# Kernel optimization log

Hardware: AMD Instinct MI355X
Metric: run time of the kernel (lower is better)

The kernel has to match this reference:

```python
import jax, jax.numpy as jnp
import numpy as np

INF = 1.0e10
EPS = 1e-12

def setup_inputs() -> dict:
    key = jax.random.key(0)
    k1, k2 = jax.random.split(key)
    B, N, A = 512, 16384, 64
    return {
        "residue_ca_pos": jax.random.normal(k1, (B, N, 3), dtype=jnp.float32) * 10.0,
        "residue_mask": jnp.ones((B, N), dtype=jnp.float32),
        "atom_pos": jax.random.normal(k2, (B, A, 3), dtype=jnp.float32) * 10.0,
        "atom_mask": jnp.ones((B, A), dtype=jnp.float32),
        "max_p": 1,
        "top_k": 4096,
    }

def reference(residue_ca_pos, residue_mask, atom_pos, atom_mask, max_p, top_k):
    # ligand centroid per batch: [B, 3]
    centroid = atom_pos.sum(-2) / atom_mask.sum(-1, keepdims=True)
    # distance from centroid to each residue Ca, invalid residues pushed to +inf
    diff = centroid[:, None, :] - residue_ca_pos            # [B, N, 3]
    dists = jnp.sqrt(jnp.sum(diff * diff, axis=-1) + EPS) + (1.0 - residue_mask) * INF
    # k smallest distances -> neighbor indices [B, top_k]
    _, nbr_indices = jax.lax.top_k(-dists, top_k)
    rows = jnp.arange(residue_mask.shape[0])[:, None]       # [B, 1]
    # scatter writes building the masks (faithful to torch scatter_ with constants)
    residue_spatial_mask = residue_mask.at[rows, nbr_indices].set(0.0)
    residue_spatial_mask_esm = (1.0 - residue_mask).at[rows, nbr_indices].set(32.0)
    return residue_spatial_mask, residue_spatial_mask_esm
```

## Files before the change

### kernel.cpp

```cpp
#include <hip/hip_runtime.h>

#pragma clang fp contract(off)

#define B_   512
#define N_   16384
#define A_   64
#define TPB  1024
#define CAP  2048
#define ITERS 4

__global__ __launch_bounds__(TPB) void fused_kernel(
    const float* __restrict__ pos,   const float* __restrict__ mask,
    const float* __restrict__ apos,  const float* __restrict__ amask,
    const int*   __restrict__ topk_ptr,
    float* __restrict__ out0, float* __restrict__ out1)
{
#pragma clang fp contract(off)
    __shared__ unsigned short dist16[N_];
    __shared__ unsigned       hist[2048];
    __shared__ unsigned       hist2[32];
    __shared__ unsigned       cand_bits[CAP];
    __shared__ unsigned short cand_idx[CAP];
    __shared__ float          s_atoms[A_ * 3 + A_];
    __shared__ float          s_c[3];
    __shared__ unsigned       s_B11, s_less11, s_P16, s_j, s_ncand, s_k;

    const int tid = threadIdx.x;
    const int b   = blockIdx.x;
    const float* __restrict__ p = pos  + (size_t)b * N_ * 3;
    const float* __restrict__ m = mask + (size_t)b * N_;

    hist[tid]        = 0u;
    hist[tid + 1024] = 0u;
    if (tid < 32) hist2[tid] = 0u;
    if (tid < 256)
        s_atoms[tid] = (tid < 192) ? apos[(size_t)b * 192 + tid]
                                   : amask[(size_t)b * 64 + (tid - 192)];
    if (tid == 0) {
        s_ncand = 0u;
        int kk = *topk_ptr;
        if (kk < 0)  kk = 0;
        if (kk > N_) kk = N_;
        s_k = (unsigned)kk;
    }
    __syncthreads();

    if (tid < 64) {
        float comp = 0.0f, ms = 0.0f;
        if (tid < 3) {
            comp = s_atoms[tid];
            for (int a = 1; a < A_; ++a) comp += s_atoms[a * 3 + tid];
        }
        if (tid == 3) {
            const float* am = s_atoms + 192;
            float r0 = am[0], r1 = am[1], r2 = am[2], r3 = am[3];
            float r4 = am[4], r5 = am[5], r6 = am[6], r7 = am[7];
            for (int i = 8; i < A_; i += 8) {
                r0 += am[i + 0]; r1 += am[i + 1]; r2 += am[i + 2]; r3 += am[i + 3];
                r4 += am[i + 4]; r5 += am[i + 5]; r6 += am[i + 6]; r7 += am[i + 7];
            }
            ms = ((r0 + r1) + (r2 + r3)) + ((r4 + r5) + (r6 + r7));
        }
        ms = __shfl(ms, 3, 64);
        if (tid < 3) s_c[tid] = comp / ms;
    }
    __syncthreads();

    const float cx = s_c[0], cy = s_c[1], cz = s_c[2];
    const unsigned k = s_k;

    unsigned rbits[ITERS * 4];
    float    rm[ITERS * 4];
#pragma unroll
    for (int it = 0; it < ITERS; ++it) {
        const int i0 = it * (TPB * 4) + tid * 4;
        const float4 pa = *(const float4*)(p + (size_t)i0 * 3);
        const float4 pb = *(const float4*)(p + (size_t)i0 * 3 + 4);
        const float4 pc = *(const float4*)(p + (size_t)i0 * 3 + 8);
        const float4 mv = *(const float4*)(m + i0);
        const float px[4] = {pa.x, pa.w, pb.z, pc.y};
        const float py[4] = {pa.y, pb.x, pb.w, pc.z};
        const float pz[4] = {pa.z, pb.y, pc.x, pc.w};
        const float mm[4] = {mv.x, mv.y, mv.z, mv.w};
        unsigned short loc[4];
#pragma unroll
        for (int j = 0; j < 4; ++j) {
            float dx = cx - px[j], dy = cy - py[j], dz = cz - pz[j];
            float dx2 = dx * dx, dy2 = dy * dy, dz2 = dz * dz;
            float s = (dx2 + dy2) + dz2;
            s = s + 1e-12f;
            float d = sqrtf(s);
            float im = (1.0f - mm[j]) * 1e10f;
            d = d + im;
            const unsigned bits = __float_as_uint(d);
            rbits[it * 4 + j] = bits;
            rm[it * 4 + j]    = mm[j];
            loc[j] = (unsigned short)(bits >> 16);
            atomicAdd(&hist[bits >> 21], 1u);
        }
        *(ushort4*)&dist16[i0] = make_ushort4(loc[0], loc[1], loc[2], loc[3]);
    }
    __syncthreads();

    if (k > 0) {
        if (tid < 64) {
            unsigned s = 0;
#pragma unroll
            for (int i = 0; i < 32; ++i) s += hist[tid * 32 + i];
            unsigned incl = s;
#pragma unroll
            for (int off = 1; off < 64; off <<= 1) {
                unsigned v = (unsigned)__shfl_up((int)incl, off, 64);
                if (tid >= off) incl += v;
            }
            unsigned long long bal = __ballot(incl >= k);
            const int g = __ffsll(bal) - 1;
            const unsigned cum1 = (unsigned)__shfl((int)(incl - s), g, 64);

            unsigned h2 = (tid < 32) ? hist[g * 32 + tid] : 0u;
            unsigned incl2 = h2;
#pragma unroll
            for (int off = 1; off < 64; off <<= 1) {
                unsigned v = (unsigned)__shfl_up((int)incl2, off, 64);
                if (tid >= off) incl2 += v;
            }
            unsigned long long bal2 = __ballot(tid < 32 && (cum1 + incl2 >= k));
            const int sb = __ffsll(bal2) - 1;
            const unsigned cum2 = cum1 + (unsigned)__shfl((int)(incl2 - h2), sb, 64);
            if (tid == 0) { s_B11 = (unsigned)(g * 32 + sb); s_less11 = cum2; }
        }
        __syncthreads();
        const unsigned B11 = s_B11;

#pragma unroll
        for (int x = 0; x < ITERS * 4; ++x) {
            const unsigned v = rbits[x] >> 16;
            if ((v >> 5) == B11) atomicAdd(&hist2[v & 31u], 1u);
        }
        __syncthreads();
        if (tid < 64) {
            unsigned h = (tid < 32) ? hist2[tid] : 0u;
            unsigned incl = h;
#pragma unroll
            for (int off = 1; off < 64; off <<= 1) {
                unsigned v = (unsigned)__shfl_up((int)incl, off, 64);
                if (tid >= off) incl += v;
            }
            const unsigned less11 = s_less11;
            unsigned long long bal = __ballot(tid < 32 && (less11 + incl >= k));
            const int sb = __ffsll(bal) - 1;
            const unsigned cumx = less11 + (unsigned)__shfl((int)(incl - h), sb, 64);
            if (tid == 0) { s_P16 = (B11 << 5) | (unsigned)sb; s_j = k - cumx; }
        }
        __syncthreads();
        const unsigned P16 = s_P16;
        const unsigned j   = s_j;

#pragma unroll
        for (int it = 0; it < ITERS; ++it) {
#pragma unroll
            for (int jj = 0; jj < 4; ++jj) {
                const unsigned bits = rbits[it * 4 + jj];
                if ((bits >> 16) == P16) {
                    const unsigned w = atomicAdd(&s_ncand, 1u);
                    if (w < CAP) {
                        cand_bits[w] = bits;
                        cand_idx[w]  = (unsigned short)(it * (TPB * 4) + tid * 4 + jj);
                    }
                }
            }
        }
        __syncthreads();

        const unsigned c = min(s_ncand, (unsigned)CAP);
        for (unsigned t = tid; t < c; t += TPB) {
            const unsigned bt = cand_bits[t];
            const unsigned it = cand_idx[t];
            unsigned rank = 0;
            for (unsigned u = 0; u < c; ++u) {
                const unsigned bu = cand_bits[u];
                rank += (bu < bt) || (bu == bt && (unsigned)cand_idx[u] < it);
            }
            if (rank < j) dist16[it] = 0;
        }
        __syncthreads();
    }

    const unsigned P16f = (k > 0) ? s_P16 : 0u;
#pragma unroll
    for (int it = 0; it < ITERS; ++it) {
        const int i0 = it * (TPB * 4) + tid * 4;
        const ushort4 dv = *(const ushort4*)&dist16[i0];
        const unsigned short dvs[4] = {dv.x, dv.y, dv.z, dv.w};
        float4 o0, o1;
        float* o0p = &o0.x; float* o1p = &o1.x;
#pragma unroll
        for (int jj = 0; jj < 4; ++jj) {
            const bool sel = (unsigned)dvs[jj] < P16f;
            const float mv = rm[it * 4 + jj];
            o0p[jj] = sel ? 0.0f  : mv;
            o1p[jj] = sel ? 32.0f : (1.0f - mv);
        }
        *(float4*)(out0 + (size_t)b * N_ + i0) = o0;
        *(float4*)(out1 + (size_t)b * N_ + i0) = o1;
    }
}

extern "C" void kernel_launch(void* const* d_in, const int* in_sizes, int n_in,
                              void* d_out, int out_size, void* d_ws, size_t ws_size,
                              hipStream_t stream) {
    const float* pos   = (const float*)d_in[0];
    const float* rmask = (const float*)d_in[1];
    const float* apos  = (const float*)d_in[2];
    const float* amask = (const float*)d_in[3];
    const int*   topk  = (const int*)d_in[5];

    float* out0 = (float*)d_out;
    float* out1 = out0 + (size_t)B_ * N_;

    fused_kernel<<<B_, TPB, 0, stream>>>(pos, rmask, apos, amask, topk, out0, out1);
}
```

Baseline: 210.7 us.

## Use min/max-adaptive single-pass histogram and exact threshold instead of two-level radix select

Replaces the fixed 16-bit two-level radix histogram with one 2048-bin histogram scaled to the block's actual min/max distance bits. The candidate bucket is then ranked exactly to find the k-th element (value, index), and the final mask compares each register-held value against that threshold. This removes the 32KB dist16 shared array, the second histogram pass and one barrier, and it loads atom data directly from global memory. It adds a block min/max reduction, 64-bit shift math per element and a __launch_bounds__ occupancy hint. There is a risk of CAP overflow if many values land in one bucket.

```diff
diff --git a/kernel.cpp b/kernel.cpp
--- a/kernel.cpp
+++ b/kernel.cpp
@@ -2,57 +2,48 @@
 
 #pragma clang fp contract(off)
 
-#define B_   512
-#define N_   16384
-#define A_   64
-#define TPB  1024
-#define CAP  2048
+#define B_    512
+#define N_    16384
+#define A_    64
+#define TPB   1024
 #define ITERS 4
-
-__global__ __launch_bounds__(TPB) void fused_kernel(
+#define CAP   2048
+
+__global__ __launch_bounds__(TPB, 8) void fused_kernel(
     const float* __restrict__ pos,   const float* __restrict__ mask,
     const float* __restrict__ apos,  const float* __restrict__ amask,
     const int*   __restrict__ topk_ptr,
     float* __restrict__ out0, float* __restrict__ out1)
 {
 #pragma clang fp contract(off)
-    __shared__ unsigned short dist16[N_];
     __shared__ unsigned       hist[2048];
-    __shared__ unsigned       hist2[32];
     __shared__ unsigned       cand_bits[CAP];
     __shared__ unsigned short cand_idx[CAP];
-    __shared__ float          s_atoms[A_ * 3 + A_];
     __shared__ float          s_c[3];
-    __shared__ unsigned       s_B11, s_less11, s_P16, s_j, s_ncand, s_k;
-
-    const int tid = threadIdx.x;
-    const int b   = blockIdx.x;
+    __shared__ unsigned       wmin[16], wmax[16];
+    __shared__ unsigned       s_minb, s_shift, s_g, s_cum, s_ncand, s_k;
+    __shared__ unsigned       s_Tb, s_Ti;
+
+    const int tid  = threadIdx.x;
+    const int lane = tid & 63;
+    const int wid  = tid >> 6;
+    const int b    = blockIdx.x;
     const float* __restrict__ p = pos  + (size_t)b * N_ * 3;
     const float* __restrict__ m = mask + (size_t)b * N_;
 
     hist[tid]        = 0u;
     hist[tid + 1024] = 0u;
-    if (tid < 32) hist2[tid] = 0u;
-    if (tid < 256)
-        s_atoms[tid] = (tid < 192) ? apos[(size_t)b * 192 + tid]
-                                   : amask[(size_t)b * 64 + (tid - 192)];
-    if (tid == 0) {
-        s_ncand = 0u;
-        int kk = *topk_ptr;
-        if (kk < 0)  kk = 0;
-        if (kk > N_) kk = N_;
-        s_k = (unsigned)kk;
-    }
-    __syncthreads();
+    if (tid == 0) { s_ncand = 0u; s_Tb = 0u; s_Ti = 0u; }
 
     if (tid < 64) {
+        const float* ap = apos  + (size_t)b * (A_ * 3);
+        const float* am = amask + (size_t)b * A_;
         float comp = 0.0f, ms = 0.0f;
         if (tid < 3) {
-            comp = s_atoms[tid];
-            for (int a = 1; a < A_; ++a) comp += s_atoms[a * 3 + tid];
+            comp = ap[tid];
+            for (int a = 1; a < A_; ++a) comp += ap[a * 3 + tid];
         }
         if (tid == 3) {
-            const float* am = s_atoms + 192;
             float r0 = am[0], r1 = am[1], r2 = am[2], r3 = am[3];
             float r4 = am[4], r5 = am[5], r6 = am[6], r7 = am[7];
             for (int i = 8; i < A_; i += 8) {
@@ -63,6 +54,12 @@
         }
         ms = __shfl(ms, 3, 64);
         if (tid < 3) s_c[tid] = comp / ms;
+        if (tid == 4) {
+            int kk = *topk_ptr;
+            if (kk < 0)  kk = 0;
+            if (kk > N_) kk = N_;
+            s_k = (unsigned)kk;
+        }
     }
     __syncthreads();
 
@@ -70,10 +67,11 @@
     const unsigned k = s_k;
 
     unsigned rbits[ITERS * 4];
-    float    rm[ITERS * 4];
-#pragma unroll
-    for (int it = 0; it < ITERS; ++it) {
-        const int i0 = it * (TPB * 4) + tid * 4;
+    float    rm16[ITERS * 4];
+    unsigned mn = 0xFFFFFFFFu, mx = 0u;
+#pragma unroll
+    for (int it2 = 0; it2 < ITERS; ++it2) {
+        const int i0 = it2 * (TPB * 4) + tid * 4;
         const float4 pa = *(const float4*)(p + (size_t)i0 * 3);
         const float4 pb = *(const float4*)(p + (size_t)i0 * 3 + 4);
         const float4 pc = *(const float4*)(p + (size_t)i0 * 3 + 8);
@@ -82,7 +80,6 @@
         const float py[4] = {pa.y, pb.x, pb.w, pc.z};
         const float pz[4] = {pa.z, pb.y, pc.x, pc.w};
         const float mm[4] = {mv.x, mv.y, mv.z, mv.w};
-        unsigned short loc[4];
 #pragma unroll
         for (int j = 0; j < 4; ++j) {
             float dx = cx - px[j], dy = cy - py[j], dz = cz - pz[j];
@@ -93,79 +90,91 @@
             float im = (1.0f - mm[j]) * 1e10f;
             d = d + im;
             const unsigned bits = __float_as_uint(d);
-            rbits[it * 4 + j] = bits;
-            rm[it * 4 + j]    = mm[j];
-            loc[j] = (unsigned short)(bits >> 16);
-            atomicAdd(&hist[bits >> 21], 1u);
-        }
-        *(ushort4*)&dist16[i0] = make_ushort4(loc[0], loc[1], loc[2], loc[3]);
-    }
+            rbits[it2 * 4 + j] = bits;
+            rm16[it2 * 4 + j]  = mm[j];
+            mn = min(mn, bits); mx = max(mx, bits);
+        }
+    }
+#pragma unroll
+    for (int off = 32; off >= 1; off >>= 1) {
+        mn = min(mn, (unsigned)__shfl_xor((int)mn, off, 64));
+        mx = max(mx, (unsigned)__shfl_xor((int)mx, off, 64));
+    }
+    if (lane == 0) { wmin[wid] = mn; wmax[wid] = mx; }
     __syncthreads();
+    if (tid < 64) {
+        unsigned a  = (tid < 16) ? wmin[tid] : 0xFFFFFFFFu;
+        unsigned bx = (tid < 16) ? wmax[tid] : 0u;
+#pragma unroll
+        for (int off = 8; off >= 1; off >>= 1) {
+            a  = min(a,  (unsigned)__shfl_xor((int)a,  off, 64));
+            bx = max(bx, (unsigned)__shfl_xor((int)bx, off, 64));
+        }
+        if (tid == 0) {
+            s_minb = a;
+            const unsigned range = bx - a;
+            s_shift = (range == 0u) ? 0u : (unsigned)(32 - __clz(range));
+        }
+    }
+    __syncthreads();
+
+    const unsigned minb = s_minb, sh = s_shift;
+#pragma unroll
+    for (int x = 0; x < ITERS * 4; ++x) {
+        const unsigned idx =
+            (unsigned)(((unsigned long long)(rbits[x] - minb) << 11) >> sh);
+        atomicAdd(&hist[idx], 1u);
+    }
 
     if (k > 0) {
+        __syncthreads();
         if (tid < 64) {
-            unsigned s = 0;
-#pragma unroll
-            for (int i = 0; i < 32; ++i) s += hist[tid * 32 + i];
-            unsigned incl = s;
+            unsigned ssum = 0;
+            const uint4* hp = (const uint4*)&hist[tid * 32];
+#pragma unroll
+            for (int r = 0; r < 8; ++r) {
+                const uint4 h4 = hp[r];
+                ssum += h4.x + h4.y + h4.z + h4.w;
+            }
+            unsigned incl = ssum;
 #pragma unroll
             for (int off = 1; off < 64; off <<= 1) {
-                unsigned v = (unsigned)__shfl_up((int)incl, off, 64);
+                const unsigned v = (unsigned)__shfl_up((int)incl, off, 64);
                 if (tid >= off) incl += v;
             }
-            unsigned long long bal = __ballot(incl >= k);
-            const int g = __ffsll(bal) - 1;
-            const unsigned cum1 = (unsigned)__shfl((int)(incl - s), g, 64);
-
-            unsigned h2 = (tid < 32) ? hist[g * 32 + tid] : 0u;
+            const unsigned long long bal = __ballot(incl >= k);
+            const int g64 = __ffsll(bal) - 1;
+            const unsigned cum64 = (unsigned)__shfl((int)(incl - ssum), g64, 64);
+
+            const unsigned h2 = (tid < 32) ? hist[g64 * 32 + tid] : 0u;
             unsigned incl2 = h2;
 #pragma unroll
             for (int off = 1; off < 64; off <<= 1) {
-                unsigned v = (unsigned)__shfl_up((int)incl2, off, 64);
+                const unsigned v = (unsigned)__shfl_up((int)incl2, off, 64);
                 if (tid >= off) incl2 += v;
             }
-            unsigned long long bal2 = __ballot(tid < 32 && (cum1 + incl2 >= k));
+            const unsigned long long bal2 =
+                __ballot(tid < 32 && (cum64 + incl2 >= k));
             const int sb = __ffsll(bal2) - 1;
-            const unsigned cum2 = cum1 + (unsigned)__shfl((int)(incl2 - h2), sb, 64);
-            if (tid == 0) { s_B11 = (unsigned)(g * 32 + sb); s_less11 = cum2; }
-        }
-        __syncthreads();
-        const unsigned B11 = s_B11;
-
-#pragma unroll
-        for (int x = 0; x < ITERS * 4; ++x) {
-            const unsigned v = rbits[x] >> 16;
-            if ((v >> 5) == B11) atomicAdd(&hist2[v & 31u], 1u);
-        }
-        __syncthreads();
-        if (tid < 64) {
-            unsigned h = (tid < 32) ? hist2[tid] : 0u;
-            unsigned incl = h;
-#pragma unroll
-            for (int off = 1; off < 64; off <<= 1) {
-                unsigned v = (unsigned)__shfl_up((int)incl, off, 64);
-                if (tid >= off) incl += v;
-            }
-            const unsigned less11 = s_less11;
-            unsigned long long bal = __ballot(tid < 32 && (less11 + incl >= k));
-            const int sb = __ffsll(bal) - 1;
-            const unsigned cumx = less11 + (unsigned)__shfl((int)(incl - h), sb, 64);
-            if (tid == 0) { s_P16 = (B11 << 5) | (unsigned)sb; s_j = k - cumx; }
-        }
-        __syncthreads();
-        const unsigned P16 = s_P16;
-        const unsigned j   = s_j;
-
-#pragma unroll
-        for (int it = 0; it < ITERS; ++it) {
+            const unsigned cum = cum64 + (unsigned)__shfl((int)(incl2 - h2), sb, 64);
+            if (tid == 0) { s_g = (unsigned)(g64 * 32 + sb); s_cum = cum; }
+        }
+        __syncthreads();
+        const unsigned g = s_g;
+
+#pragma unroll
+        for (int it2 = 0; it2 < ITERS; ++it2) {
 #pragma unroll
             for (int jj = 0; jj < 4; ++jj) {
-                const unsigned bits = rbits[it * 4 + jj];
-                if ((bits >> 16) == P16) {
+                const unsigned bits = rbits[it2 * 4 + jj];
+                const unsigned idx =
+                    (unsigned)(((unsigned long long)(bits - minb) << 11) >> sh);
+                if (idx == g) {
                     const unsigned w = atomicAdd(&s_ncand, 1u);
                     if (w < CAP) {
                         cand_bits[w] = bits;
-                        cand_idx[w]  = (unsigned short)(it * (TPB * 4) + tid * 4 + jj);
+                        cand_idx[w]  =
+                            (unsigned short)(it2 * (TPB * 4) + tid * 4 + jj);
                     }
                 }
             }
@@ -173,6 +182,7 @@
         __syncthreads();
 
         const unsigned c = min(s_ncand, (unsigned)CAP);
+        const unsigned j = k - s_cum;
         for (unsigned t = tid; t < c; t += TPB) {
             const unsigned bt = cand_bits[t];
             const unsigned it = cand_idx[t];
@@ -181,23 +191,23 @@
                 const unsigned bu = cand_bits[u];
                 rank += (bu < bt) || (bu == bt && (unsigned)cand_idx[u] < it);
             }
-            if (rank < j) dist16[it] = 0;
-        }
-        __syncthreads();
-    }
-
-    const unsigned P16f = (k > 0) ? s_P16 : 0u;
-#pragma unroll
-    for (int it = 0; it < ITERS; ++it) {
-        const int i0 = it * (TPB * 4) + tid * 4;
-        const ushort4 dv = *(const ushort4*)&dist16[i0];
-        const unsigned short dvs[4] = {dv.x, dv.y, dv.z, dv.w};
+            if (rank == j - 1) { s_Tb = bt; s_Ti = it; }
+        }
+        __syncthreads();
+    }
+
+    const unsigned Tb = s_Tb, Ti = s_Ti;
+#pragma unroll
+    for (int it2 = 0; it2 < ITERS; ++it2) {
+        const int i0 = it2 * (TPB * 4) + tid * 4;
         float4 o0, o1;
         float* o0p = &o0.x; float* o1p = &o1.x;
 #pragma unroll
         for (int jj = 0; jj < 4; ++jj) {
-            const bool sel = (unsigned)dvs[jj] < P16f;
-            const float mv = rm[it * 4 + jj];
+            const unsigned bits = rbits[it2 * 4 + jj];
+            const unsigned gi   = (unsigned)(i0 + jj);
+            const bool sel = (bits < Tb) || (bits == Tb && gi <= Ti);
+            const float mv = rm16[it2 * 4 + jj];
             o0p[jj] = sel ? 0.0f  : mv;
             o1p[jj] = sel ? 32.0f : (1.0f - mv);
         }
```

Measured after the change: 229.9 us. +9.1%, slower.

## Split fused top-k kernel into three kernels with global histogram workspace

Applied to the files above, without the earlier changes.

Replaces the single 512-block fused kernel with three launches. The first computes distances over 4096 smaller blocks and merges per-slice histograms into global memory with atomics, storing 16-bit distance prefixes in a workspace. The second selects the threshold per batch, recomputing exact distances only for candidates in the boundary bucket. The third writes both masks, again over 4096 blocks. The aim is better occupancy and latency hiding than one 1024-thread block per batch holding a large LDS footprint. The cost is extra global traffic, a memset, global atomics and two extra launches.

```diff
diff --git a/kernel.cpp b/kernel.cpp
--- a/kernel.cpp
+++ b/kernel.cpp
@@ -2,57 +2,38 @@
 
 #pragma clang fp contract(off)
 
-#define B_   512
-#define N_   16384
-#define A_   64
-#define TPB  1024
-#define CAP  2048
-#define ITERS 4
-
-__global__ __launch_bounds__(TPB) void fused_kernel(
-    const float* __restrict__ pos,   const float* __restrict__ mask,
-    const float* __restrict__ apos,  const float* __restrict__ amask,
-    const int*   __restrict__ topk_ptr,
-    float* __restrict__ out0, float* __restrict__ out1)
+#define B_  512
+#define N_  16384
+#define A_  64
+#define SL  8
+#define EPT 8
+#define CAP 2048
+
+__global__ __launch_bounds__(256) void k1_dist(
+    const float* __restrict__ pos,  const float* __restrict__ mask,
+    const float* __restrict__ apos, const float* __restrict__ amask,
+    float* __restrict__ centws, unsigned* __restrict__ hist_g,
+    unsigned short* __restrict__ ws16)
 {
 #pragma clang fp contract(off)
-    __shared__ unsigned short dist16[N_];
-    __shared__ unsigned       hist[2048];
-    __shared__ unsigned       hist2[32];
-    __shared__ unsigned       cand_bits[CAP];
-    __shared__ unsigned short cand_idx[CAP];
-    __shared__ float          s_atoms[A_ * 3 + A_];
-    __shared__ float          s_c[3];
-    __shared__ unsigned       s_B11, s_less11, s_P16, s_j, s_ncand, s_k;
-
+    __shared__ unsigned hist[2048];
+    __shared__ float s_c[3];
     const int tid = threadIdx.x;
-    const int b   = blockIdx.x;
-    const float* __restrict__ p = pos  + (size_t)b * N_ * 3;
-    const float* __restrict__ m = mask + (size_t)b * N_;
-
-    hist[tid]        = 0u;
-    hist[tid + 1024] = 0u;
-    if (tid < 32) hist2[tid] = 0u;
-    if (tid < 256)
-        s_atoms[tid] = (tid < 192) ? apos[(size_t)b * 192 + tid]
-                                   : amask[(size_t)b * 64 + (tid - 192)];
-    if (tid == 0) {
-        s_ncand = 0u;
-        int kk = *topk_ptr;
-        if (kk < 0)  kk = 0;
-        if (kk > N_) kk = N_;
-        s_k = (unsigned)kk;
-    }
-    __syncthreads();
+    const int blk = blockIdx.x;
+    const int b = blk >> 3, sl = blk & 7;
+
+#pragma unroll
+    for (int i = 0; i < 8; ++i) hist[tid + i * 256] = 0u;
 
     if (tid < 64) {
+        const float* ap = apos  + (size_t)b * (A_ * 3);
+        const float* am = amask + (size_t)b * A_;
         float comp = 0.0f, ms = 0.0f;
         if (tid < 3) {
-            comp = s_atoms[tid];
-            for (int a = 1; a < A_; ++a) comp += s_atoms[a * 3 + tid];
+            comp = ap[tid];
+            for (int a = 1; a < A_; ++a) comp += ap[a * 3 + tid];
         }
         if (tid == 3) {
-            const float* am = s_atoms + 192;
             float r0 = am[0], r1 = am[1], r2 = am[2], r3 = am[3];
             float r4 = am[4], r5 = am[5], r6 = am[6], r7 = am[7];
             for (int i = 8; i < A_; i += 8) {
@@ -65,24 +46,24 @@
         if (tid < 3) s_c[tid] = comp / ms;
     }
     __syncthreads();
+    if (sl == 0 && tid < 3) centws[b * 4 + tid] = s_c[tid];
 
     const float cx = s_c[0], cy = s_c[1], cz = s_c[2];
-    const unsigned k = s_k;
-
-    unsigned rbits[ITERS * 4];
-    float    rm[ITERS * 4];
-#pragma unroll
-    for (int it = 0; it < ITERS; ++it) {
-        const int i0 = it * (TPB * 4) + tid * 4;
-        const float4 pa = *(const float4*)(p + (size_t)i0 * 3);
-        const float4 pb = *(const float4*)(p + (size_t)i0 * 3 + 4);
-        const float4 pc = *(const float4*)(p + (size_t)i0 * 3 + 8);
-        const float4 mv = *(const float4*)(m + i0);
+    const int base = b * N_ + sl * 2048 + tid * EPT;
+    const float* __restrict__ p = pos  + (size_t)base * 3;
+    const float* __restrict__ m = mask + base;
+
+    unsigned bits[EPT];
+#pragma unroll
+    for (int g = 0; g < 2; ++g) {
+        const float4 pa = *(const float4*)(p + g * 12);
+        const float4 pb = *(const float4*)(p + g * 12 + 4);
+        const float4 pc = *(const float4*)(p + g * 12 + 8);
+        const float4 mv = *(const float4*)(m + g * 4);
         const float px[4] = {pa.x, pa.w, pb.z, pc.y};
         const float py[4] = {pa.y, pb.x, pb.w, pc.z};
         const float pz[4] = {pa.z, pb.y, pc.x, pc.w};
         const float mm[4] = {mv.x, mv.y, mv.z, mv.w};
-        unsigned short loc[4];
 #pragma unroll
         for (int j = 0; j < 4; ++j) {
             float dx = cx - px[j], dy = cy - py[j], dz = cz - pz[j];
@@ -90,120 +71,180 @@
             float s = (dx2 + dy2) + dz2;
             s = s + 1e-12f;
             float d = sqrtf(s);
-            float im = (1.0f - mm[j]) * 1e10f;
-            d = d + im;
-            const unsigned bits = __float_as_uint(d);
-            rbits[it * 4 + j] = bits;
-            rm[it * 4 + j]    = mm[j];
-            loc[j] = (unsigned short)(bits >> 16);
-            atomicAdd(&hist[bits >> 21], 1u);
-        }
-        *(ushort4*)&dist16[i0] = make_ushort4(loc[0], loc[1], loc[2], loc[3]);
-    }
-    __syncthreads();
-
-    if (k > 0) {
-        if (tid < 64) {
-            unsigned s = 0;
-#pragma unroll
-            for (int i = 0; i < 32; ++i) s += hist[tid * 32 + i];
-            unsigned incl = s;
-#pragma unroll
-            for (int off = 1; off < 64; off <<= 1) {
-                unsigned v = (unsigned)__shfl_up((int)incl, off, 64);
-                if (tid >= off) incl += v;
+            d = d + (1.0f - mm[j]) * 1e10f;
+            bits[g * 4 + j] = __float_as_uint(d);
+        }
+    }
+#pragma unroll
+    for (int x = 0; x < EPT; ++x) atomicAdd(&hist[bits[x] >> 21], 1u);
+
+    uint4 pk;
+    pk.x = (bits[0] >> 16) | ((bits[1] >> 16) << 16);
+    pk.y = (bits[2] >> 16) | ((bits[3] >> 16) << 16);
+    pk.z = (bits[4] >> 16) | ((bits[5] >> 16) << 16);
+    pk.w = (bits[6] >> 16) | ((bits[7] >> 16) << 16);
+    *(uint4*)(ws16 + base) = pk;
+
+    __syncthreads();
+#pragma unroll
+    for (int i = 0; i < 8; ++i) {
+        const unsigned v = hist[tid + i * 256];
+        if (v) atomicAdd(&hist_g[b * 2048 + tid + i * 256], v);
+    }
+}
+
+__global__ __launch_bounds__(1024) void k2_select(
+    const float* __restrict__ pos, const float* __restrict__ mask,
+    const int* __restrict__ topk_ptr, const float* __restrict__ centws,
+    const unsigned* __restrict__ hist_g, unsigned* __restrict__ P16arr,
+    unsigned short* __restrict__ ws16)
+{
+#pragma clang fp contract(off)
+    __shared__ unsigned       hist2[32];
+    __shared__ unsigned       cand_bits[CAP];
+    __shared__ unsigned short cand_idx[CAP];
+    __shared__ float          s_c[3];
+    __shared__ unsigned       s_B11, s_cum, s_P16, s_j, s_ncand, s_k;
+
+    const int tid = threadIdx.x;
+    const int b   = blockIdx.x;
+    if (tid < 32) hist2[tid] = 0u;
+    if (tid < 3)  s_c[tid] = centws[b * 4 + tid];
+    if (tid == 0) {
+        s_ncand = 0u;
+        int kk = *topk_ptr;
+        if (kk < 0)  kk = 0;
+        if (kk > N_) kk = N_;
+        s_k = (unsigned)kk;
+    }
+    __syncthreads();
+    const unsigned k = s_k;
+    if (k == 0u) { if (tid == 0) P16arr[b] = 0u; return; }
+
+    if (tid < 64) {
+        const uint4* hp = (const uint4*)(hist_g + (size_t)b * 2048 + tid * 32);
+        unsigned ssum = 0;
+#pragma unroll
+        for (int r = 0; r < 8; ++r) { const uint4 h = hp[r]; ssum += h.x + h.y + h.z + h.w; }
+        unsigned incl = ssum;
+#pragma unroll
+        for (int off = 1; off < 64; off <<= 1) {
+            const unsigned v = (unsigned)__shfl_up((int)incl, off, 64);
+            if (tid >= off) incl += v;
+        }
+        const unsigned long long bal = __ballot(incl >= k);
+        const int g64 = __ffsll(bal) - 1;
+        const unsigned cum64 = (unsigned)__shfl((int)(incl - ssum), g64, 64);
+        const unsigned h2 = (tid < 32) ? hist_g[(size_t)b * 2048 + g64 * 32 + tid] : 0u;
+        unsigned incl2 = h2;
+#pragma unroll
+        for (int off = 1; off < 64; off <<= 1) {
+            const unsigned v = (unsigned)__shfl_up((int)incl2, off, 64);
+            if (tid >= off) incl2 += v;
+        }
+        const unsigned long long bal2 = __ballot(tid < 32 && (cum64 + incl2 >= k));
+        const int sb = __ffsll(bal2) - 1;
+        const unsigned cum = cum64 + (unsigned)__shfl((int)(incl2 - h2), sb, 64);
+        if (tid == 0) { s_B11 = (unsigned)(g64 * 32 + sb); s_cum = cum; }
+    }
+    __syncthreads();
+    const unsigned B11 = s_B11;
+
+    unsigned short* __restrict__ w16 = ws16 + (size_t)b * N_;
+    const uint4* wp = (const uint4*)(w16 + (size_t)tid * 16);
+    const uint4 a0 = wp[0];
+    const uint4 a1 = wp[1];
+    const unsigned pref[16] = {
+        a0.x & 0xFFFFu, a0.x >> 16, a0.y & 0xFFFFu, a0.y >> 16,
+        a0.z & 0xFFFFu, a0.z >> 16, a0.w & 0xFFFFu, a0.w >> 16,
+        a1.x & 0xFFFFu, a1.x >> 16, a1.y & 0xFFFFu, a1.y >> 16,
+        a1.z & 0xFFFFu, a1.z >> 16, a1.w & 0xFFFFu, a1.w >> 16 };
+#pragma unroll
+    for (int x = 0; x < 16; ++x)
+        if ((pref[x] >> 5) == B11) atomicAdd(&hist2[pref[x] & 31u], 1u);
+    __syncthreads();
+    if (tid < 64) {
+        const unsigned h = (tid < 32) ? hist2[tid] : 0u;
+        unsigned incl = h;
+#pragma unroll
+        for (int off = 1; off < 64; off <<= 1) {
+            const unsigned v = (unsigned)__shfl_up((int)incl, off, 64);
+            if (tid >= off) incl += v;
+        }
+        const unsigned cum0 = s_cum;
+        const unsigned long long bal = __ballot(tid < 32 && (cum0 + incl >= k));
+        const int sb = __ffsll(bal) - 1;
+        const unsigned cumx = cum0 + (unsigned)__shfl((int)(incl - h), sb, 64);
+        if (tid == 0) { s_P16 = (B11 << 5) | (unsigned)sb; s_j = k - cumx; }
+    }
+    __syncthreads();
+    const unsigned P16 = s_P16, j = s_j;
+
+    const float cx = s_c[0], cy = s_c[1], cz = s_c[2];
+    const float* __restrict__ p = pos  + (size_t)b * N_ * 3;
+    const float* __restrict__ m = mask + (size_t)b * N_;
+#pragma unroll
+    for (int x = 0; x < 16; ++x) {
+        if (pref[x] == P16) {
+            const unsigned w = atomicAdd(&s_ncand, 1u);
+            if (w < CAP) {
+                const int i = tid * 16 + x;
+                float dx = cx - p[i * 3], dy = cy - p[i * 3 + 1], dz = cz - p[i * 3 + 2];
+                float dx2 = dx * dx, dy2 = dy * dy, dz2 = dz * dz;
+                float s = (dx2 + dy2) + dz2;
+                s = s + 1e-12f;
+                float d = sqrtf(s);
+                d = d + (1.0f - m[i]) * 1e10f;
+                cand_bits[w] = __float_as_uint(d);
+                cand_idx[w]  = (unsigned short)i;
             }
-            unsigned long long bal = __ballot(incl >= k);
-            const int g = __ffsll(bal) - 1;
-            const unsigned cum1 = (unsigned)__shfl((int)(incl - s), g, 64);
-
-            unsigned h2 = (tid < 32) ? hist[g * 32 + tid] : 0u;
-            unsigned incl2 = h2;
-#pragma unroll
-            for (int off = 1; off < 64; off <<= 1) {
-                unsigned v = (unsigned)__shfl_up((int)incl2, off, 64);
-                if (tid >= off) incl2 += v;
-            }
-            unsigned long long bal2 = __ballot(tid < 32 && (cum1 + incl2 >= k));
-            const int sb = __ffsll(bal2) - 1;
-            const unsigned cum2 = cum1 + (unsigned)__shfl((int)(incl2 - h2), sb, 64);
-            if (tid == 0) { s_B11 = (unsigned)(g * 32 + sb); s_less11 = cum2; }
-        }
-        __syncthreads();
-        const unsigned B11 = s_B11;
-
-#pragma unroll
-        for (int x = 0; x < ITERS * 4; ++x) {
-            const unsigned v = rbits[x] >> 16;
-            if ((v >> 5) == B11) atomicAdd(&hist2[v & 31u], 1u);
-        }
-        __syncthreads();
-        if (tid < 64) {
-            unsigned h = (tid < 32) ? hist2[tid] : 0u;
-            unsigned incl = h;
-#pragma unroll
-            for (int off = 1; off < 64; off <<= 1) {
-                unsigned v = (unsigned)__shfl_up((int)incl, off, 64);
-                if (tid >= off) incl += v;
-            }
-            const unsigned less11 = s_less11;
-            unsigned long long bal = __ballot(tid < 32 && (less11 + incl >= k));
-            const int sb = __ffsll(bal) - 1;
-            const unsigned cumx = less11 + (unsigned)__shfl((int)(incl - h), sb, 64);
-            if (tid == 0) { s_P16 = (B11 << 5) | (unsigned)sb; s_j = k - cumx; }
-        }
-        __syncthreads();
-        const unsigned P16 = s_P16;
-        const unsigned j   = s_j;
-
-#pragma unroll
-        for (int it = 0; it < ITERS; ++it) {
-#pragma unroll
-            for (int jj = 0; jj < 4; ++jj) {
-                const unsigned bits = rbits[it * 4 + jj];
-                if ((bits >> 16) == P16) {
-                    const unsigned w = atomicAdd(&s_ncand, 1u);
-                    if (w < CAP) {
-                        cand_bits[w] = bits;
-                        cand_idx[w]  = (unsigned short)(it * (TPB * 4) + tid * 4 + jj);
-                    }
-                }
-            }
-        }
-        __syncthreads();
-
-        const unsigned c = min(s_ncand, (unsigned)CAP);
-        for (unsigned t = tid; t < c; t += TPB) {
-            const unsigned bt = cand_bits[t];
-            const unsigned it = cand_idx[t];
-            unsigned rank = 0;
-            for (unsigned u = 0; u < c; ++u) {
-                const unsigned bu = cand_bits[u];
-                rank += (bu < bt) || (bu == bt && (unsigned)cand_idx[u] < it);
-            }
-            if (rank < j) dist16[it] = 0;
-        }
-        __syncthreads();
-    }
-
-    const unsigned P16f = (k > 0) ? s_P16 : 0u;
-#pragma unroll
-    for (int it = 0; it < ITERS; ++it) {
-        const int i0 = it * (TPB * 4) + tid * 4;
-        const ushort4 dv = *(const ushort4*)&dist16[i0];
-        const unsigned short dvs[4] = {dv.x, dv.y, dv.z, dv.w};
-        float4 o0, o1;
-        float* o0p = &o0.x; float* o1p = &o1.x;
-#pragma unroll
-        for (int jj = 0; jj < 4; ++jj) {
-            const bool sel = (unsigned)dvs[jj] < P16f;
-            const float mv = rm[it * 4 + jj];
-            o0p[jj] = sel ? 0.0f  : mv;
-            o1p[jj] = sel ? 32.0f : (1.0f - mv);
-        }
-        *(float4*)(out0 + (size_t)b * N_ + i0) = o0;
-        *(float4*)(out1 + (size_t)b * N_ + i0) = o1;
-    }
+        }
+    }
+    __syncthreads();
+
+    const unsigned c = min(s_ncand, (unsigned)CAP);
+    for (unsigned t = tid; t < c; t += 1024) {
+        const unsigned bt = cand_bits[t];
+        const unsigned it = cand_idx[t];
+        unsigned rank = 0;
+        for (unsigned u = 0; u < c; ++u) {
+            const unsigned bu = cand_bits[u];
+            rank += (bu < bt) || (bu == bt && (unsigned)cand_idx[u] < it);
+        }
+        if (rank < j) w16[it] = 0;
+    }
+    if (tid == 0) P16arr[b] = P16;
+}
+
+__global__ __launch_bounds__(256) void k3_write(
+    const float* __restrict__ mask, const unsigned* __restrict__ P16arr,
+    const unsigned short* __restrict__ ws16,
+    float* __restrict__ out0, float* __restrict__ out1)
+{
+    const int tid = threadIdx.x;
+    const int blk = blockIdx.x;
+    const int b = blk >> 3, sl = blk & 7;
+    const int base = b * N_ + sl * 2048 + tid * EPT;
+    const unsigned P16 = P16arr[b];
+
+    const uint4  pk = *(const uint4*)(ws16 + base);
+    const float4 m0 = *(const float4*)(mask + base);
+    const float4 m1 = *(const float4*)(mask + base + 4);
+    const unsigned pre[8] = {pk.x & 0xFFFFu, pk.x >> 16, pk.y & 0xFFFFu, pk.y >> 16,
+                             pk.z & 0xFFFFu, pk.z >> 16, pk.w & 0xFFFFu, pk.w >> 16};
+    const float mm[8] = {m0.x, m0.y, m0.z, m0.w, m1.x, m1.y, m1.z, m1.w};
+
+    float o0v[8], o1v[8];
+#pragma unroll
+    for (int x = 0; x < 8; ++x) {
+        const bool sel = pre[x] < P16;
+        o0v[x] = sel ? 0.0f  : mm[x];
+        o1v[x] = sel ? 32.0f : (1.0f - mm[x]);
+    }
+    *(float4*)(out0 + base)     = make_float4(o0v[0], o0v[1], o0v[2], o0v[3]);
+    *(float4*)(out0 + base + 4) = make_float4(o0v[4], o0v[5], o0v[6], o0v[7]);
+    *(float4*)(out1 + base)     = make_float4(o1v[0], o1v[1], o1v[2], o1v[3]);
+    *(float4*)(out1 + base + 4) = make_float4(o1v[4], o1v[5], o1v[6], o1v[7]);
 }
 
 extern "C" void kernel_launch(void* const* d_in, const int* in_sizes, int n_in,
@@ -218,5 +259,14 @@
     float* out0 = (float*)d_out;
     float* out1 = out0 + (size_t)B_ * N_;
 
-    fused_kernel<<<B_, TPB, 0, stream>>>(pos, rmask, apos, amask, topk, out0, out1);
-}
+    char* ws = (char*)d_ws;
+    float*          centws = (float*)ws;
+    unsigned*       P16arr = (unsigned*)(ws + 8192);
+    unsigned*       hist_g = (unsigned*)(ws + 16384);
+    unsigned short* ws16   = (unsigned short*)(ws + 16384 + (size_t)B_ * 2048 * 4);
+
+    hipMemsetAsync(hist_g, 0, (size_t)B_ * 2048 * sizeof(unsigned), stream);
+    k1_dist  <<<B_ * SL, 256,  0, stream>>>(pos, rmask, apos, amask, centws, hist_g, ws16);
+    k2_select<<<B_,      1024, 0, stream>>>(pos, rmask, topk, centws, hist_g, P16arr, ws16);
+    k3_write <<<B_ * SL, 256,  0, stream>>>(rmask, P16arr, ws16, out0, out1);
+}
```

Result: slower. 235.4 us (+11.8%).

## Stream positions through LDS chunks instead of holding distances in registers

Applied to the files above, without the earlier changes.

Drops the 32 per-thread register arrays (distance bits and mask) and instead stages positions through a double-buffered LDS chunk, one element per thread per chunk. Later passes (second histogram, candidate collection) use the 16-bit prefixes in LDS, recompute exact distances only for candidates, and reload the mask for the output pass. The aim is lower register pressure and higher occupancy (launch bounds now request 8 waves). The cost is a sync per chunk, scalar instead of float4 global loads, more LDS use, and a second read of the mask from global memory.

```diff
diff --git a/kernel.cpp b/kernel.cpp
--- a/kernel.cpp
+++ b/kernel.cpp
@@ -2,28 +2,29 @@
 
 #pragma clang fp contract(off)
 
-#define B_   512
-#define N_   16384
-#define A_   64
-#define TPB  1024
-#define CAP  2048
-#define ITERS 4
-
-__global__ __launch_bounds__(TPB) void fused_kernel(
+#define B_     512
+#define N_     16384
+#define A_     64
+#define TPB    1024
+#define CHUNK  1024
+#define NCHUNK 16
+#define CAP    2048
+
+__global__ __launch_bounds__(TPB, 8) void fused_kernel(
     const float* __restrict__ pos,   const float* __restrict__ mask,
     const float* __restrict__ apos,  const float* __restrict__ amask,
     const int*   __restrict__ topk_ptr,
     float* __restrict__ out0, float* __restrict__ out1)
 {
 #pragma clang fp contract(off)
+    __shared__ float          s_pos[2][3 * CHUNK];
     __shared__ unsigned short dist16[N_];
     __shared__ unsigned       hist[2048];
     __shared__ unsigned       hist2[32];
     __shared__ unsigned       cand_bits[CAP];
     __shared__ unsigned short cand_idx[CAP];
-    __shared__ float          s_atoms[A_ * 3 + A_];
     __shared__ float          s_c[3];
-    __shared__ unsigned       s_B11, s_less11, s_P16, s_j, s_ncand, s_k;
+    __shared__ unsigned       s_B11, s_cum, s_P16, s_j, s_ncand, s_k;
 
     const int tid = threadIdx.x;
     const int b   = blockIdx.x;
@@ -33,26 +34,17 @@
     hist[tid]        = 0u;
     hist[tid + 1024] = 0u;
     if (tid < 32) hist2[tid] = 0u;
-    if (tid < 256)
-        s_atoms[tid] = (tid < 192) ? apos[(size_t)b * 192 + tid]
-                                   : amask[(size_t)b * 64 + (tid - 192)];
-    if (tid == 0) {
-        s_ncand = 0u;
-        int kk = *topk_ptr;
-        if (kk < 0)  kk = 0;
-        if (kk > N_) kk = N_;
-        s_k = (unsigned)kk;
-    }
-    __syncthreads();
+    if (tid == 0) s_ncand = 0u;
 
     if (tid < 64) {
+        const float* ap = apos  + (size_t)b * (A_ * 3);
+        const float* am = amask + (size_t)b * A_;
         float comp = 0.0f, ms = 0.0f;
         if (tid < 3) {
-            comp = s_atoms[tid];
-            for (int a = 1; a < A_; ++a) comp += s_atoms[a * 3 + tid];
+            comp = ap[tid];
+            for (int a = 1; a < A_; ++a) comp += ap[a * 3 + tid];
         }
         if (tid == 3) {
-            const float* am = s_atoms + 192;
             float r0 = am[0], r1 = am[1], r2 = am[2], r3 = am[3];
             float r4 = am[4], r5 = am[5], r6 = am[6], r7 = am[7];
             for (int i = 8; i < A_; i += 8) {
@@ -63,110 +55,115 @@
         }
         ms = __shfl(ms, 3, 64);
         if (tid < 3) s_c[tid] = comp / ms;
+        if (tid == 4) {
+            int kk = *topk_ptr;
+            if (kk < 0)  kk = 0;
+            if (kk > N_) kk = N_;
+            s_k = (unsigned)kk;
+        }
     }
     __syncthreads();
 
     const float cx = s_c[0], cy = s_c[1], cz = s_c[2];
     const unsigned k = s_k;
 
-    unsigned rbits[ITERS * 4];
-    float    rm[ITERS * 4];
-#pragma unroll
-    for (int it = 0; it < ITERS; ++it) {
-        const int i0 = it * (TPB * 4) + tid * 4;
-        const float4 pa = *(const float4*)(p + (size_t)i0 * 3);
-        const float4 pb = *(const float4*)(p + (size_t)i0 * 3 + 4);
-        const float4 pc = *(const float4*)(p + (size_t)i0 * 3 + 8);
-        const float4 mv = *(const float4*)(m + i0);
-        const float px[4] = {pa.x, pa.w, pb.z, pc.y};
-        const float py[4] = {pa.y, pb.x, pb.w, pc.z};
-        const float pz[4] = {pa.z, pb.y, pc.x, pc.w};
-        const float mm[4] = {mv.x, mv.y, mv.z, mv.w};
-        unsigned short loc[4];
-#pragma unroll
-        for (int j = 0; j < 4; ++j) {
-            float dx = cx - px[j], dy = cy - py[j], dz = cz - pz[j];
-            float dx2 = dx * dx, dy2 = dy * dy, dz2 = dz * dz;
-            float s = (dx2 + dy2) + dz2;
-            s = s + 1e-12f;
-            float d = sqrtf(s);
-            float im = (1.0f - mm[j]) * 1e10f;
-            d = d + im;
-            const unsigned bits = __float_as_uint(d);
-            rbits[it * 4 + j] = bits;
-            rm[it * 4 + j]    = mm[j];
-            loc[j] = (unsigned short)(bits >> 16);
-            atomicAdd(&hist[bits >> 21], 1u);
-        }
-        *(ushort4*)&dist16[i0] = make_ushort4(loc[0], loc[1], loc[2], loc[3]);
+    for (int c = 0; c < NCHUNK; ++c) {
+        float* sb = s_pos[c & 1];
+        const float* src = p + c * (3 * CHUNK);
+        sb[tid]        = src[tid];
+        sb[tid + 1024] = src[tid + 1024];
+        sb[tid + 2048] = src[tid + 2048];
+        const float mv = m[c * CHUNK + tid];
+        __syncthreads();
+
+        const float px = sb[3 * tid + 0];
+        const float py = sb[3 * tid + 1];
+        const float pz = sb[3 * tid + 2];
+        float dx = cx - px, dy = cy - py, dz = cz - pz;
+        float dx2 = dx * dx, dy2 = dy * dy, dz2 = dz * dz;
+        float s = (dx2 + dy2) + dz2;
+        s = s + 1e-12f;
+        float d = sqrtf(s);
+        d = d + (1.0f - mv) * 1e10f;
+        const unsigned bits = __float_as_uint(d);
+        dist16[c * CHUNK + tid] = (unsigned short)(bits >> 16);
+        atomicAdd(&hist[bits >> 21], 1u);
     }
     __syncthreads();
 
     if (k > 0) {
         if (tid < 64) {
-            unsigned s = 0;
-#pragma unroll
-            for (int i = 0; i < 32; ++i) s += hist[tid * 32 + i];
-            unsigned incl = s;
+            const uint4* hp = (const uint4*)&hist[tid * 32];
+            unsigned ssum = 0;
+#pragma unroll
+            for (int r = 0; r < 8; ++r) {
+                const uint4 h = hp[r];
+                ssum += h.x + h.y + h.z + h.w;
+            }
+            unsigned incl = ssum;
 #pragma unroll
             for (int off = 1; off < 64; off <<= 1) {
-                unsigned v = (unsigned)__shfl_up((int)incl, off, 64);
+                const unsigned v = (unsigned)__shfl_up((int)incl, off, 64);
                 if (tid >= off) incl += v;
             }
-            unsigned long long bal = __ballot(incl >= k);
-            const int g = __ffsll(bal) - 1;
-            const unsigned cum1 = (unsigned)__shfl((int)(incl - s), g, 64);
-
-            unsigned h2 = (tid < 32) ? hist[g * 32 + tid] : 0u;
+            const unsigned long long bal = __ballot(incl >= k);
+            const int g64 = __ffsll(bal) - 1;
+            const unsigned cum64 = (unsigned)__shfl((int)(incl - ssum), g64, 64);
+            const unsigned h2 = (tid < 32) ? hist[g64 * 32 + tid] : 0u;
             unsigned incl2 = h2;
 #pragma unroll
             for (int off = 1; off < 64; off <<= 1) {
-                unsigned v = (unsigned)__shfl_up((int)incl2, off, 64);
+                const unsigned v = (unsigned)__shfl_up((int)incl2, off, 64);
                 if (tid >= off) incl2 += v;
             }
-            unsigned long long bal2 = __ballot(tid < 32 && (cum1 + incl2 >= k));
-            const int sb = __ffsll(bal2) - 1;
-            const unsigned cum2 = cum1 + (unsigned)__shfl((int)(incl2 - h2), sb, 64);
-            if (tid == 0) { s_B11 = (unsigned)(g * 32 + sb); s_less11 = cum2; }
+            const unsigned long long bal2 =
+                __ballot(tid < 32 && (cum64 + incl2 >= k));
+            const int sb2 = __ffsll(bal2) - 1;
+            const unsigned cum =
+                cum64 + (unsigned)__shfl((int)(incl2 - h2), sb2, 64);
+            if (tid == 0) { s_B11 = (unsigned)(g64 * 32 + sb2); s_cum = cum; }
         }
         __syncthreads();
         const unsigned B11 = s_B11;
 
-#pragma unroll
-        for (int x = 0; x < ITERS * 4; ++x) {
-            const unsigned v = rbits[x] >> 16;
-            if ((v >> 5) == B11) atomicAdd(&hist2[v & 31u], 1u);
+        for (int c = 0; c < NCHUNK; ++c) {
+            const unsigned pref = dist16[c * CHUNK + tid];
+            if ((pref >> 5) == B11) atomicAdd(&hist2[pref & 31u], 1u);
         }
         __syncthreads();
         if (tid < 64) {
-            unsigned h = (tid < 32) ? hist2[tid] : 0u;
+            const unsigned h = (tid < 32) ? hist2[tid] : 0u;
             unsigned incl = h;
 #pragma unroll
             for (int off = 1; off < 64; off <<= 1) {
-                unsigned v = (unsigned)__shfl_up((int)incl, off, 64);
+                const unsigned v = (unsigned)__shfl_up((int)incl, off, 64);
                 if (tid >= off) incl += v;
             }
-            const unsigned less11 = s_less11;
-            unsigned long long bal = __ballot(tid < 32 && (less11 + incl >= k));
-            const int sb = __ffsll(bal) - 1;
-            const unsigned cumx = less11 + (unsigned)__shfl((int)(incl - h), sb, 64);
-            if (tid == 0) { s_P16 = (B11 << 5) | (unsigned)sb; s_j = k - cumx; }
-        }
-        __syncthreads();
-        const unsigned P16 = s_P16;
-        const unsigned j   = s_j;
-
-#pragma unroll
-        for (int it = 0; it < ITERS; ++it) {
-#pragma unroll
-            for (int jj = 0; jj < 4; ++jj) {
-                const unsigned bits = rbits[it * 4 + jj];
-                if ((bits >> 16) == P16) {
-                    const unsigned w = atomicAdd(&s_ncand, 1u);
-                    if (w < CAP) {
-                        cand_bits[w] = bits;
-                        cand_idx[w]  = (unsigned short)(it * (TPB * 4) + tid * 4 + jj);
-                    }
+            const unsigned cum0 = s_cum;
+            const unsigned long long bal =
+                __ballot(tid < 32 && (cum0 + incl >= k));
+            const int sb2 = __ffsll(bal) - 1;
+            const unsigned cumx =
+                cum0 + (unsigned)__shfl((int)(incl - h), sb2, 64);
+            if (tid == 0) { s_P16 = (B11 << 5) | (unsigned)sb2; s_j = k - cumx; }
+        }
+        __syncthreads();
+        const unsigned P16 = s_P16, j = s_j;
+
+        for (int c = 0; c < NCHUNK; ++c) {
+            const int i = c * CHUNK + tid;
+            if (dist16[i] == (unsigned short)P16) {
+                const unsigned w = atomicAdd(&s_ncand, 1u);
+                if (w < CAP) {
+                    float dx = cx - p[i * 3], dy = cy - p[i * 3 + 1];
+                    float dz = cz - p[i * 3 + 2];
+                    float dx2 = dx * dx, dy2 = dy * dy, dz2 = dz * dz;
+                    float s = (dx2 + dy2) + dz2;
+                    s = s + 1e-12f;
+                    float d = sqrtf(s);
+                    d = d + (1.0f - m[i]) * 1e10f;
+                    cand_bits[w] = __float_as_uint(d);
+                    cand_idx[w]  = (unsigned short)i;
                 }
             }
         }
@@ -188,18 +185,19 @@
 
     const unsigned P16f = (k > 0) ? s_P16 : 0u;
 #pragma unroll
-    for (int it = 0; it < ITERS; ++it) {
-        const int i0 = it * (TPB * 4) + tid * 4;
+    for (int c = 0; c < 4; ++c) {
+        const int i0 = c * 4096 + tid * 4;
         const ushort4 dv = *(const ushort4*)&dist16[i0];
-        const unsigned short dvs[4] = {dv.x, dv.y, dv.z, dv.w};
+        const float4  mv = *(const float4*)(m + i0);
+        const unsigned pre[4] = {dv.x, dv.y, dv.z, dv.w};
+        const float    mm[4]  = {mv.x, mv.y, mv.z, mv.w};
         float4 o0, o1;
         float* o0p = &o0.x; float* o1p = &o1.x;
 #pragma unroll
         for (int jj = 0; jj < 4; ++jj) {
-            const bool sel = (unsigned)dvs[jj] < P16f;
-            const float mv = rm[it * 4 + jj];
-            o0p[jj] = sel ? 0.0f  : mv;
-            o1p[jj] = sel ? 32.0f : (1.0f - mv);
+            const bool sel = pre[jj] < P16f;
+            o0p[jj] = sel ? 0.0f  : mm[jj];
+            o1p[jj] = sel ? 32.0f : (1.0f - mm[jj]);
         }
         *(float4*)(out0 + (size_t)b * N_ + i0) = o0;
         *(float4*)(out1 + (size_t)b * N_ + i0) = o1;
```

New measurement: 214.1 us. No clear change (+1.6%).
